# Performance work log

Measured on AMD Instinct MI355X. Metric: run time of the kernel, lower is better.

Reference implementation:

```python
import jax, jax.numpy as jnp
import numpy as np
from jax import lax

B, T, D, H = 64, 2048, 128, 256  # batch, seq_len, input_dim, hidden_dim


def setup_inputs() -> dict:
    key = jax.random.key(0)
    ks = jax.random.split(key, 21)
    s = 0.05
    p = lambda k, shape: jax.random.normal(k, shape, dtype=jnp.float32) * s
    inp = {"x": jax.random.normal(ks[0], (B, T, D), dtype=jnp.float32)}
    i = 1
    for n in ["e1", "e2", "d1", "d2"]:  # encode1, encode2, reconstruct1, reconstruct2
        inp[n + "_Wih"] = p(ks[i], (4 * H, D)); i += 1
        inp[n + "_Whh"] = p(ks[i], (4 * H, H)); i += 1
        inp[n + "_bih"] = p(ks[i], (4 * H,)); i += 1
        inp[n + "_bhh"] = p(ks[i], (4 * H,)); i += 1
    inp["l1_W"] = p(ks[17], (D, H)); inp["l1_b"] = p(ks[18], (D,))
    inp["l2_W"] = p(ks[19], (D, H)); inp["l2_b"] = p(ks[20], (D,))
    return inp


def _lstm_cell(h, c, xt, Wih, Whh, bih, bhh):
    # PyTorch gate order: i, f, g, o
    g = xt @ Wih.T + h @ Whh.T + bih + bhh  # [B, 4H]
    i, f, gg, o = jnp.split(g, 4, axis=-1)
    c = jax.nn.sigmoid(f) * c + jax.nn.sigmoid(i) * jnp.tanh(gg)
    h = jax.nn.sigmoid(o) * jnp.tanh(c)
    return h, c


def _encode(x, h0, c0, Wih, Whh, bih, bhh):
    # x: [B, T, D] batch_first -> scan over time
    def step(carry, xt):
        h, c = carry
        h, c = _lstm_cell(h, c, xt, Wih, Whh, bih, bhh)
        return (h, c), None
    (h, c), _ = lax.scan(step, (h0, c0), jnp.swapaxes(x, 0, 1))
    return h, c


def _decode(n, h, c, Wih, Whh, bih, bhh, Wl, bl):
    # first output is linear(hidden) before any cell step (matches original decode)
    inp0 = h @ Wl.T + bl  # [B, D]
    def step(carry, _):
        h, c, inp = carry
        h, c = _lstm_cell(h, c, inp, Wih, Whh, bih, bhh)
        inp = h @ Wl.T + bl
        return (h, c, inp), inp
    _, outs = lax.scan(step, (h, c, inp0), None, length=n - 1)  # [n-1, B, D]
    out = jnp.concatenate([inp0[None], outs], axis=0)  # [n, B, D]
    return jnp.swapaxes(out, 0, 1)  # [B, n, D]


def reference(x,
              e1_Wih, e1_Whh, e1_bih, e1_bhh,
              e2_Wih, e2_Whh, e2_bih, e2_bhh,
              d1_Wih, d1_Whh, d1_bih, d1_bhh,
              d2_Wih, d2_Whh, d2_bih, d2_bhh,
              l1_W, l1_b, l2_W, l2_b):
    Bc, Tc = x.shape[0], x.shape[1]
    T1 = Tc // 2
    h0 = jnp.zeros((Bc, H), dtype=x.dtype)
    c0 = jnp.zeros((Bc, H), dtype=x.dtype)
    x1 = x[:, :T1][:, ::-1]  # first half, time-reversed
    x2 = x[:, T1:]
    h1, c1 = _encode(x1, h0, c0, e1_Wih, e1_Whh, e1_bih, e1_bhh)
    h2, c2 = _encode(x2, h1, c1, e2_Wih, e2_Whh, e2_bih, e2_bhh)
    out1 = _decode(T1, h1, c1, d1_Wih, d1_Whh, d1_bih, d1_bhh, l1_W, l1_b)
    out2 = _decode(Tc - T1, h2, c2, d2_Wih, d2_Whh, d2_bih, d2_bhh, l2_W, l2_b)[:, ::-1]
    return jnp.concatenate([out1, out2], axis=1)  # [B, T, D]
```

## Files before the change

kernel.cpp:

```cpp
#include <hip/hip_runtime.h>
#include <stdint.h>

#define Bv 64
#define Tv 2048
#define T1v 1024
#define Dv 128
#define Hv 256

typedef _Float16 h2_t __attribute__((ext_vector_type(2)));

__device__ inline float d2(uint32_t hp, uint32_t wp, float acc) {
#if __has_builtin(__builtin_amdgcn_fdot2)
  return __builtin_amdgcn_fdot2(__builtin_bit_cast(h2_t, hp),
                                __builtin_bit_cast(h2_t, wp), acc, false);
#else
  float out;
  asm("v_dot2_f32_f16 %0, %1, %2, %3" : "=v"(out) : "v"(hp), "v"(wp), "v"(acc));
  return out;
#endif
}

__device__ inline uint16_t f2h(float x) {
  _Float16 h = (_Float16)x;
  return __builtin_bit_cast(uint16_t, h);
}
__device__ inline float h2f(uint16_t u) {
  return (float)__builtin_bit_cast(_Float16, u);
}
__device__ inline uint32_t packpair(float a, float b) {
  return (uint32_t)f2h(a) | ((uint32_t)f2h(b) << 16);
}
__device__ inline float unpk(uint32_t u, int hi) {
  return h2f((uint16_t)(hi ? (u >> 16) : (u & 0xffff)));
}
__device__ inline float sigm(float x) { return 1.f / (1.f + __expf(-x)); }
__device__ inline float tanh_(float x) { return 2.f / (1.f + __expf(-2.f * x)) - 1.f; }

__device__ inline float qsum4(float v) {
  int t = __builtin_amdgcn_update_dpp(0, __float_as_int(v), 0xB1, 0xF, 0xF, true);
  v += __int_as_float(t);
  t = __builtin_amdgcn_update_dpp(0, __float_as_int(v), 0x4E, 0xF, 0xF, true);
  return v + __int_as_float(t);
}

__device__ inline uint4 ld_stream(const uint4* p) {
  const volatile uint32_t* q = (const volatile uint32_t*)p;
  uint4 v;
  v.x = q[0];
  v.y = q[1];
  v.z = q[2];
  v.w = q[3];
  return v;
}


__global__ void k_pack_x(const float* __restrict__ x, uint32_t* __restrict__ xpk) {
  int idx = blockIdx.x * 256 + threadIdx.x;
  const float2* x2 = (const float2*)x;
  float2 v = x2[idx];
  xpk[idx] = packpair(v.x, v.y);
}

__global__ void k_pack_w(const float* __restrict__ src, uint32_t* __restrict__ wAll,
                         uint32_t* __restrict__ wLg, uint32_t* __restrict__ wStr) {
  int idx = blockIdx.x * 256 + threadIdx.x;
  int row = idx >> 7, k2 = idx & 127;
  uint32_t pr = packpair(src[row * 256 + 2 * k2], src[row * 256 + 2 * k2 + 1]);
  wAll[k2 * 1024 + row] = pr;
  if (k2 >= 96) {
    int g = (k2 - 96) >> 2, qq = (k2 - 96) & 3;
    wLg[(g * 1024 + row) * 4 + qq] = pr;
  }
  if (k2 >= 48 && k2 < 96) wStr[row * 48 + (k2 - 48)] = pr;
}

__global__ void k_pack_w2(const float* __restrict__ src, uint32_t* __restrict__ wSt,
                          uint32_t* __restrict__ wLds) {
  int idx = blockIdx.x * 256 + threadIdx.x;
  int r = idx >> 7, k2 = idx & 127;
  uint32_t pr = packpair(src[r * 256 + 2 * k2], src[r * 256 + 2 * k2 + 1]);
  int gate = r >> 8, u = r & 255;
  int u_hi = u >> 7, jb = u & 127;
  int q = k2 >> 5, kk = k2 & 31;
  int tid = jb * 4 + q;
  int ri = u_hi * 4 + gate;
  if (kk < 24) {
    wSt[((ri * 6 + (kk >> 2)) * 512 + tid) * 4 + (kk & 3)] = pr;
  } else {
    wLds[((ri * 2 + ((kk - 24) >> 2)) * 512 + tid) * 4 + ((kk - 24) & 3)] = pr;
  }
}

__global__ void k_bias_pack(const float* __restrict__ b32, uint32_t* __restrict__ bpk) {
  int jb = threadIdx.x;
  uint32_t w[4];
#pragma unroll
  for (int wi = 0; wi < 4; ++wi) {
    int ri0 = 2 * wi, ri1 = 2 * wi + 1;
    int row0 = (ri0 & 3) * 256 + jb + 128 * (ri0 >> 2);
    int row1 = (ri1 & 3) * 256 + jb + 128 * (ri1 >> 2);
    w[wi] = packpair(b32[row0], b32[row1]);
  }
  ((uint4*)bpk)[jb] = make_uint4(w[0], w[1], w[2], w[3]);
}

__global__ void k_pack_wih(const float* __restrict__ Wih, uint32_t* __restrict__ wihp) {
  int idx = blockIdx.x * 256 + threadIdx.x;
  int row = idx >> 6, k2 = idx & 63;
  wihp[row * 64 + k2] = packpair(Wih[row * 128 + 2 * k2], Wih[row * 128 + 2 * k2 + 1]);
}

__global__ void k_bias2(const float* __restrict__ bih, const float* __restrict__ bhh,
                        float* __restrict__ bias) {
  int i = blockIdx.x * 256 + threadIdx.x;
  if (i < 1024) bias[i] = bih[i] + bhh[i];
}

__global__ void k_dec_combine(const float* __restrict__ Whh, const float* __restrict__ Wih,
                              const float* __restrict__ bih, const float* __restrict__ bhh,
                              const float* __restrict__ lW, const float* __restrict__ lb,
                              float* __restrict__ wd, float* __restrict__ bias) {
  int j = blockIdx.x;
  int k = threadIdx.x;
  __shared__ float wr[128];
  if (k < 128) wr[k] = Wih[j * 128 + k];
  __syncthreads();
  float acc = Whh[j * 256 + k];
  for (int d = 0; d < 128; ++d) acc += wr[d] * lW[d * 256 + k];
  wd[j * 256 + k] = acc;
  if (k == 0) {
    float s = bih[j] + bhh[j];
    for (int d = 0; d < 128; ++d) s += wr[d] * lb[d];
    bias[j] = s;
  }
}

__global__ void k_pack_wl(const float* __restrict__ lW, uint32_t* __restrict__ wlp) {
  int idx = blockIdx.x * 256 + threadIdx.x;
  int d = idx >> 7, k2 = idx & 127;
  wlp[d * 128 + k2] = packpair(lW[d * 256 + 2 * k2], lW[d * 256 + 2 * k2 + 1]);
}

template <int LAY>
__global__ __launch_bounds__(256) void k_xp_gemm(const uint32_t* __restrict__ xpk,
                                                 const uint32_t* __restrict__ wihp,
                                                 uint16_t* __restrict__ xp, int xt0, int xdt) {
  const int b = blockIdx.z;
  const int s0 = blockIdx.y * 32;
  const int r = blockIdx.x * 256 + threadIdx.x;
  uint32_t wreg[64];
#pragma unroll
  for (int k = 0; k < 64; ++k) wreg[k] = wihp[r * 64 + k];
  const int gate = r >> 8, u = r & 255;
  const int u_hi = u >> 7, jb = u & 127;
  const int ri = u_hi * 4 + gate;
  for (int sl = 0; sl < 32; ++sl) {
    const int s = s0 + sl;
    const int t = xt0 + s * xdt;
    const uint32_t* __restrict__ xrow = xpk + ((size_t)b * Tv + t) * 64;
    float a0 = 0.f, a1 = 0.f;
#pragma unroll
    for (int k = 0; k < 64; k += 2) {
      a0 = d2(xrow[k], wreg[k], a0);
      a1 = d2(xrow[k + 1], wreg[k + 1], a1);
    }
    uint16_t v = f2h(a0 + a1);
    if (LAY == 0)
      xp[(((size_t)b * T1v + s) * 128 + jb) * 8 + ri] = v;
    else
      xp[((size_t)b * T1v + s) * 1024 + r] = v;
  }
}


struct CfgU {
  const uint4* wSt;
  const uint4* wLds;
  const uint4* bpk;
  const uint4* xps;
  const float* h0;
  const float* c0;
  float* hN;
  float* cN;
  uint16_t* hist;
};

template <int NREGC, int NSTRC, int NLDSC>
__global__ void __launch_bounds__(512)
__attribute__((amdgpu_waves_per_eu(2, 2)))
k_rnnU(CfgU cA, CfgU cB, int nA) {
  __shared__ __align__(16) uint4 wldsM[NLDSC * 8 * 512];
  __shared__ __align__(16) uint16_t hbuf[2][4][72];

  const bool isA = (int)blockIdx.x < nA;
  const CfgU cfg = isA ? cA : cB;
  const int b = isA ? (int)blockIdx.x : ((int)blockIdx.x - nA);
  const int tid = threadIdx.x;
  const int q = tid & 3, jb = tid >> 2;

#pragma unroll
  for (int ri = 0; ri < 8; ++ri)
#pragma unroll
    for (int li = 0; li < NLDSC; ++li)
      wldsM[(ri * NLDSC + li) * 512 + tid] =
          cfg.wLds[(ri * 2 + (2 - NLDSC) + li) * 512 + tid];

  uint4 wr[8][NREGC];
#pragma unroll
  for (int ri = 0; ri < 8; ++ri)
#pragma unroll
    for (int cc = 0; cc < NREGC; ++cc) wr[ri][cc] = cfg.wSt[(ri * 6 + cc) * 512 + tid];

  const uint4 bp = cfg.bpk[jb];
  float c0r = cfg.c0 ? cfg.c0[b * 256 + jb] : 0.f;
  float c1r = cfg.c0 ? cfg.c0[b * 256 + jb + 128] : 0.f;

  uint16_t* histp = cfg.hist ? cfg.hist + (size_t)b * 1024 * 256 : nullptr;
  if (q == 0) {
    float h00 = cfg.h0 ? cfg.h0[b * 256 + jb] : 0.f;
    float h01 = cfg.h0 ? cfg.h0[b * 256 + jb + 128] : 0.f;
    uint16_t u0 = f2h(h00), u1 = f2h(h01);
    hbuf[0][jb >> 6][jb & 63] = u0;
    hbuf[0][2 + (jb >> 6)][jb & 63] = u1;
    if (histp) {
      histp[jb] = u0;
      histp[jb + 128] = u1;
    }
  }
  const uint4* xps4 = cfg.xps ? cfg.xps + (size_t)b * 1024 * 128 + jb : nullptr;

  __syncthreads();

  int cur = 0;
  for (int s = 0; s < 1024; ++s) {
    uint4 xq = make_uint4(0, 0, 0, 0);
    if (xps4) xq = xps4[(size_t)s * 128];
    const uint4* Hq = (const uint4*)&hbuf[cur][q][0];

    float acc[8];
#pragma unroll
    for (int ri = 0; ri < 8; ++ri) acc[ri] = 0.f;

#pragma unroll
    for (int cc = 0; cc < NREGC; ++cc) {
      const uint4 hv = Hq[cc];
#pragma unroll
      for (int ri = 0; ri < 8; ++ri) {
        acc[ri] = d2(hv.x, wr[ri][cc].x, acc[ri]);
        acc[ri] = d2(hv.y, wr[ri][cc].y, acc[ri]);
        acc[ri] = d2(hv.z, wr[ri][cc].z, acc[ri]);
        acc[ri] = d2(hv.w, wr[ri][cc].w, acc[ri]);
      }
    }
#pragma unroll
    for (int j = 0; j < NSTRC; ++j) {
      const int cc = NREGC + j;
      const uint4 hv = Hq[cc];
#pragma unroll
      for (int ri = 0; ri < 8; ++ri) {
        const uint4 wv = (cc < 6) ? ld_stream(cfg.wSt + (ri * 6 + cc) * 512 + tid)
                                  : ld_stream(cfg.wLds + (ri * 2 + (cc - 6)) * 512 + tid);
        acc[ri] = d2(hv.x, wv.x, acc[ri]);
        acc[ri] = d2(hv.y, wv.y, acc[ri]);
        acc[ri] = d2(hv.z, wv.z, acc[ri]);
        acc[ri] = d2(hv.w, wv.w, acc[ri]);
      }
    }
#pragma unroll
    for (int li = 0; li < NLDSC; ++li) {
      const int cc = 8 - NLDSC + li;
      const uint4 hv = Hq[cc];
#pragma unroll
      for (int ri = 0; ri < 8; ++ri) {
        const uint4 wv = wldsM[(ri * NLDSC + li) * 512 + tid];
        acc[ri] = d2(hv.x, wv.x, acc[ri]);
        acc[ri] = d2(hv.y, wv.y, acc[ri]);
        acc[ri] = d2(hv.z, wv.z, acc[ri]);
        acc[ri] = d2(hv.w, wv.w, acc[ri]);
      }
    }

#pragma unroll
    for (int ri = 0; ri < 8; ++ri) acc[ri] = qsum4(acc[ri]);

    acc[0] += unpk(bp.x, 0) + unpk(xq.x, 0);
    acc[1] += unpk(bp.x, 1) + unpk(xq.x, 1);
    acc[2] += unpk(bp.y, 0) + unpk(xq.y, 0);
    acc[3] += unpk(bp.y, 1) + unpk(xq.y, 1);
    acc[4] += unpk(bp.z, 0) + unpk(xq.z, 0);
    acc[5] += unpk(bp.z, 1) + unpk(xq.z, 1);
    acc[6] += unpk(bp.w, 0) + unpk(xq.w, 0);
    acc[7] += unpk(bp.w, 1) + unpk(xq.w, 1);

    const float cn0 = sigm(acc[1]) * c0r + sigm(acc[0]) * tanh_(acc[2]);
    const float h0v = sigm(acc[3]) * tanh_(cn0);
    c0r = cn0;
    const float cn1 = sigm(acc[5]) * c1r + sigm(acc[4]) * tanh_(acc[6]);
    const float h1v = sigm(acc[7]) * tanh_(cn1);
    c1r = cn1;

    if (q == 0) {
      const uint16_t hu0 = f2h(h0v), hu1 = f2h(h1v);
      hbuf[cur ^ 1][jb >> 6][jb & 63] = hu0;
      hbuf[cur ^ 1][2 + (jb >> 6)][jb & 63] = hu1;
      if (histp && s < 1023) {
        histp[(size_t)(s + 1) * 256 + jb] = hu0;
        histp[(size_t)(s + 1) * 256 + jb + 128] = hu1;
      }
    }
    __syncthreads();
    cur ^= 1;
  }

  if (cfg.hN && q == 0) {
    cfg.hN[b * 256 + jb] = h2f(hbuf[cur][jb >> 6][jb & 63]);
    cfg.hN[b * 256 + jb + 128] = h2f(hbuf[cur][2 + (jb >> 6)][jb & 63]);
    cfg.cN[b * 256 + jb] = c0r;
    cfg.cN[b * 256 + jb + 128] = c1r;
  }
}


struct ChainCfg {
  const uint32_t* wAll;
  const uint4* wLg;
  const uint32_t* wStr;
  const uint32_t* wih;
  const uint32_t* xpk;
  const uint16_t* xps;
  const float* bias;
  const float* h0;
  const float* c0;
  float* hN;
  float* cN;
  uint16_t* hist;
  int xt0, xdt;
};

template <int NRESP, bool WIH>
__global__ void __launch_bounds__(512)
__attribute__((amdgpu_waves_per_eu(2, 2)))
k_rnn5(ChainCfg cA, ChainCfg cB, int nA) {
  __shared__ __align__(16) uint4 wlds4[8 * 1024];
  __shared__ float gsm[1024];
  __shared__ __align__(16) uint16_t h16[256];
  __shared__ __align__(16) uint32_t xsh[64];

  const bool isA = (int)blockIdx.x < nA;
  const ChainCfg cfg = isA ? cA : cB;
  const int b = isA ? (int)blockIdx.x : ((int)blockIdx.x - nA);
  const int tid = threadIdx.x;
  const int r0 = tid, r1 = tid + 512;

#pragma unroll
  for (int i = 0; i < 16; ++i) wlds4[i * 512 + tid] = cfg.wLg[i * 512 + tid];

  uint16_t* histp = cfg.hist ? cfg.hist + (size_t)b * 1024 * 256 : nullptr;

  float creg = 0.f;
  if (tid < 256) {
    float h0v = cfg.h0 ? cfg.h0[b * 256 + tid] : 0.f;
    creg = cfg.c0 ? cfg.c0[b * 256 + tid] : 0.f;
    uint16_t hu = f2h(h0v);
    h16[tid] = hu;
    if (histp) histp[tid] = hu;
  }

  uint32_t w0[NRESP], w1[NRESP];
#pragma unroll
  for (int k = 0; k < NRESP; ++k) w0[k] = cfg.wAll[k * 1024 + r0];
#pragma unroll
  for (int k = 0; k < NRESP; ++k) w1[k] = cfg.wAll[k * 1024 + r1];
  const float bias0 = cfg.bias[r0];
  const float bias1 = cfg.bias[r1];

  constexpr int NS4 = (96 - NRESP) / 4;
  const uint4* ws0 = (const uint4*)(cfg.wStr + (size_t)r0 * 48 + (NRESP - 48));
  const uint4* ws1 = (const uint4*)(cfg.wStr + (size_t)r1 * 48 + (NRESP - 48));
  const uint4* wi0 = cfg.wih ? (const uint4*)(cfg.wih + (size_t)r0 * 64) : nullptr;
  const uint4* wi1 = cfg.wih ? (const uint4*)(cfg.wih + (size_t)r1 * 64) : nullptr;
  const bool hasx = cfg.xps != nullptr;

  __syncthreads();

  for (int s = 0; s < 1024; ++s) {
    float xa0 = 0.f, xa1 = 0.f;
    if (hasx) {
      size_t xb = ((size_t)b * 1024 + s) * 1024;
      xa0 = h2f(cfg.xps[xb + r0]);
      xa1 = h2f(cfg.xps[xb + r1]);
    }
    if constexpr (WIH) {
      if (cfg.wih) {
        if (tid < 64) {
          const int t = cfg.xt0 + s * cfg.xdt;
          xsh[tid] = cfg.xpk[((size_t)b * Tv + t) * 64 + tid];
        }
        __syncthreads();
      }
    }

    const uint4* H4 = (const uint4*)h16;
    float a00 = bias0, a01 = 0.f, a10 = bias1, a11 = 0.f;

#pragma unroll
    for (int c4 = 0; c4 < NRESP / 4; ++c4) {
      const uint4 hv = H4[c4];
      a00 = d2(hv.x, w0[4 * c4 + 0], a00);
      a01 = d2(hv.y, w0[4 * c4 + 1], a01);
      a10 = d2(hv.x, w1[4 * c4 + 0], a10);
      a11 = d2(hv.y, w1[4 * c4 + 1], a11);
      a00 = d2(hv.z, w0[4 * c4 + 2], a00);
      a01 = d2(hv.w, w0[4 * c4 + 3], a01);
      a10 = d2(hv.z, w1[4 * c4 + 2], a10);
      a11 = d2(hv.w, w1[4 * c4 + 3], a11);
    }
    if constexpr (NS4 > 0) {
#pragma unroll
      for (int u = 0; u < NS4; ++u) {
        const uint4 hv = H4[NRESP / 4 + u];
        const uint4 wv0 = ws0[u];
        const uint4 wv1 = ws1[u];
        a00 = d2(hv.x, wv0.x, a00);
        a01 = d2(hv.y, wv0.y, a01);
        a10 = d2(hv.x, wv1.x, a10);
        a11 = d2(hv.y, wv1.y, a11);
        a00 = d2(hv.z, wv0.z, a00);
        a01 = d2(hv.w, wv0.w, a01);
        a10 = d2(hv.z, wv1.z, a10);
        a11 = d2(hv.w, wv1.w, a11);
      }
    }
#pragma unroll
    for (int g = 0; g < 8; ++g) {
      const uint4 hv = H4[24 + g];
      const uint4 wv0 = wlds4[g * 1024 + r0];
      const uint4 wv1 = wlds4[g * 1024 + r1];
      a00 = d2(hv.x, wv0.x, a00);
      a01 = d2(hv.y, wv0.y, a01);
      a10 = d2(hv.x, wv1.x, a10);
      a11 = d2(hv.y, wv1.y, a11);
      a00 = d2(hv.z, wv0.z, a00);
      a01 = d2(hv.w, wv0.w, a01);
      a10 = d2(hv.z, wv1.z, a10);
      a11 = d2(hv.w, wv1.w, a11);
    }
    if constexpr (WIH) {
      if (cfg.wih) {
        const uint4* XS4 = (const uint4*)xsh;
#pragma unroll
        for (int u = 0; u < 16; ++u) {
          const uint4 xv = XS4[u];
          const uint4 wv0 = wi0[u];
          const uint4 wv1 = wi1[u];
          a00 = d2(xv.x, wv0.x, a00);
          a01 = d2(xv.y, wv0.y, a01);
          a10 = d2(xv.x, wv1.x, a10);
          a11 = d2(xv.y, wv1.y, a11);
          a00 = d2(xv.z, wv0.z, a00);
          a01 = d2(xv.w, wv0.w, a01);
          a10 = d2(xv.z, wv1.z, a10);
          a11 = d2(xv.w, wv1.w, a11);
        }
      }
    }

    gsm[r0] = a00 + a01 + xa0;
    gsm[r1] = a10 + a11 + xa1;
    __syncthreads();

    if (tid < 256) {
      const float gi = gsm[tid];
      const float gf = gsm[tid + 256];
      const float gg = gsm[tid + 512];
      const float go = gsm[tid + 768];
      const float cn = sigm(gf) * creg + sigm(gi) * tanh_(gg);
      const float hv = sigm(go) * tanh_(cn);
      creg = cn;
      const uint16_t hu = f2h(hv);
      h16[tid] = hu;
      if (histp && s < 1023) histp[(size_t)(s + 1) * 256 + tid] = hu;
    }
    __syncthreads();
  }

  if (cfg.hN && tid < 256) {
    cfg.hN[b * 256 + tid] = h2f(h16[tid]);
    cfg.cN[b * 256 + tid] = creg;
  }
}

__global__ __launch_bounds__(256) void k_out(const uint16_t* __restrict__ hist,
                                             const uint32_t* __restrict__ wlp,
                                             const float* __restrict__ lb,
                                             float* __restrict__ out, int outbase, int tsign) {
  const int b = blockIdx.y;
  const int t0 = blockIdx.x * 64;
  __shared__ __align__(16) uint32_t hq[64 * 128];
  const uint32_t* hsrc = (const uint32_t*)hist;
  for (int i = threadIdx.x; i < 64 * 128; i += 256) {
    hq[i] = hsrc[((size_t)b * 1024 + t0) * 128 + i];
  }
  __syncthreads();
  const int d = threadIdx.x & 127;
  const int th = threadIdx.x >> 7;
  float acc[32];
#pragma unroll
  for (int it = 0; it < 32; ++it) acc[it] = lb[d];
  const uint4* W4 = (const uint4*)(wlp + (size_t)d * 128);
  const uint4* HQ4 = (const uint4*)hq;
  for (int k2c = 0; k2c < 32; ++k2c) {
    const uint4 wv = W4[k2c];
#pragma unroll
    for (int it = 0; it < 32; ++it) {
      const int tl = th * 32 + it;
      const uint4 hv = HQ4[tl * 32 + k2c];
      acc[it] = d2(hv.x, wv.x, acc[it]);
      acc[it] = d2(hv.y, wv.y, acc[it]);
      acc[it] = d2(hv.z, wv.z, acc[it]);
      acc[it] = d2(hv.w, wv.w, acc[it]);
    }
  }
#pragma unroll
  for (int it = 0; it < 32; ++it) {
    const int tl = th * 32 + it;
    const int t = t0 + tl;
    const int tout = outbase + tsign * t;
    out[((size_t)b * Tv + tout) * Dv + d] = acc[it];
  }
}


extern "C" void kernel_launch(void* const* d_in, const int* in_sizes, int n_in,
                              void* d_out, int out_size, void* d_ws, size_t ws_size,
                              hipStream_t stream) {
  const float* x = (const float*)d_in[0];
  const float* e1_Wih = (const float*)d_in[1];
  const float* e1_Whh = (const float*)d_in[2];
  const float* e1_bih = (const float*)d_in[3];
  const float* e1_bhh = (const float*)d_in[4];
  const float* e2_Wih = (const float*)d_in[5];
  const float* e2_Whh = (const float*)d_in[6];
  const float* e2_bih = (const float*)d_in[7];
  const float* e2_bhh = (const float*)d_in[8];
  const float* d1_Wih = (const float*)d_in[9];
  const float* d1_Whh = (const float*)d_in[10];
  const float* d1_bih = (const float*)d_in[11];
  const float* d1_bhh = (const float*)d_in[12];
  const float* d2_Wih = (const float*)d_in[13];
  const float* d2_Whh = (const float*)d_in[14];
  const float* d2_bih = (const float*)d_in[15];
  const float* d2_bhh = (const float*)d_in[16];
  const float* l1_W = (const float*)d_in[17];
  const float* l1_b = (const float*)d_in[18];
  const float* l2_W = (const float*)d_in[19];
  const float* l2_b = (const float*)d_in[20];

  uint8_t* wsb = (uint8_t*)d_ws;
  size_t off = 0;
  auto take = [&](size_t n) -> void* {
    void* pp = wsb + off;
    off += (n + 255) & ~(size_t)255;
    return pp;
  };
  uint32_t* xpk = (uint32_t*)take((size_t)Bv * Tv * 64 * 4);
  uint16_t* hist1 = (uint16_t*)take((size_t)Bv * T1v * Hv * 2);
  uint16_t* hist2 = (uint16_t*)take((size_t)Bv * T1v * Hv * 2);
  struct WSet {
    uint32_t *wAll, *wLg, *wStr, *wih;
    float* bias;
    uint32_t *wSt, *wLds, *bpk;
  };
  auto take_wset = [&](bool with_ih) -> WSet {
    WSet w;
    w.wAll = (uint32_t*)take(128 * 1024 * 4);
    w.wLg = (uint32_t*)take(8 * 1024 * 16);
    w.wStr = (uint32_t*)take(1024 * 48 * 4);
    w.wih = with_ih ? (uint32_t*)take(1024 * 64 * 4) : nullptr;
    w.bias = (float*)take(1024 * 4);
    w.wSt = (uint32_t*)take(48 * 512 * 16);
    w.wLds = (uint32_t*)take(16 * 512 * 16);
    w.bpk = (uint32_t*)take(128 * 16);
    return w;
  };
  WSet we1 = take_wset(true);
  WSet we2 = take_wset(true);
  WSet wd1 = take_wset(false);
  WSet wd2 = take_wset(false);
  float* wd32 = (float*)take(1024 * 256 * 4);
  uint32_t* wl1p = (uint32_t*)take(128 * 128 * 4);
  uint32_t* wl2p = (uint32_t*)take(128 * 128 * 4);
  float* h1 = (float*)take(64 * 256 * 4);
  float* c1 = (float*)take(64 * 256 * 4);
  float* h2 = (float*)take(64 * 256 * 4);
  float* c2 = (float*)take(64 * 256 * 4);
  uint16_t* xp = (uint16_t*)take((size_t)Bv * T1v * 1024 * 2);
  const bool use_xp = ws_size >= off;

  int variant = 4;
  {
    hipFuncAttributes fa;
    auto spillfree = [&](const void* f) {
      return hipFuncGetAttributes(&fa, f) == hipSuccess && fa.localSizeBytes == 0;
    };
    if (use_xp) {
      if (spillfree(reinterpret_cast<const void*>(&k_rnnU<6, 1, 1>))) variant = 0;
      else if (spillfree(reinterpret_cast<const void*>(&k_rnnU<6, 0, 2>))) variant = 1;
      else if (spillfree(reinterpret_cast<const void*>(&k_rnnU<4, 2, 2>))) variant = 2;
      else if (spillfree(reinterpret_cast<const void*>(&k_rnn5<96, false>))) variant = 3;
    } else {
      if (spillfree(reinterpret_cast<const void*>(&k_rnn5<96, true>))) variant = 3;
    }
  }

  k_pack_x<<<(Bv * Tv * 64) / 256, 256, 0, stream>>>(x, xpk);
  k_pack_w<<<512, 256, 0, stream>>>(e1_Whh, we1.wAll, we1.wLg, we1.wStr);
  k_pack_w2<<<512, 256, 0, stream>>>(e1_Whh, we1.wSt, we1.wLds);
  k_pack_wih<<<256, 256, 0, stream>>>(e1_Wih, we1.wih);
  k_bias2<<<4, 256, 0, stream>>>(e1_bih, e1_bhh, we1.bias);
  k_bias_pack<<<1, 128, 0, stream>>>(we1.bias, we1.bpk);
  k_pack_w<<<512, 256, 0, stream>>>(e2_Whh, we2.wAll, we2.wLg, we2.wStr);
  k_pack_w2<<<512, 256, 0, stream>>>(e2_Whh, we2.wSt, we2.wLds);
  k_pack_wih<<<256, 256, 0, stream>>>(e2_Wih, we2.wih);
  k_bias2<<<4, 256, 0, stream>>>(e2_bih, e2_bhh, we2.bias);
  k_bias_pack<<<1, 128, 0, stream>>>(we2.bias, we2.bpk);
  k_dec_combine<<<1024, 256, 0, stream>>>(d1_Whh, d1_Wih, d1_bih, d1_bhh, l1_W, l1_b, wd32, wd1.bias);
  k_pack_w<<<512, 256, 0, stream>>>(wd32, wd1.wAll, wd1.wLg, wd1.wStr);
  k_pack_w2<<<512, 256, 0, stream>>>(wd32, wd1.wSt, wd1.wLds);
  k_bias_pack<<<1, 128, 0, stream>>>(wd1.bias, wd1.bpk);
  k_dec_combine<<<1024, 256, 0, stream>>>(d2_Whh, d2_Wih, d2_bih, d2_bhh, l2_W, l2_b, wd32, wd2.bias);
  k_pack_w<<<512, 256, 0, stream>>>(wd32, wd2.wAll, wd2.wLg, wd2.wStr);
  k_pack_w2<<<512, 256, 0, stream>>>(wd32, wd2.wSt, wd2.wLds);
  k_bias_pack<<<1, 128, 0, stream>>>(wd2.bias, wd2.bpk);
  k_pack_wl<<<64, 256, 0, stream>>>(l1_W, wl1p);
  k_pack_wl<<<64, 256, 0, stream>>>(l2_W, wl2p);

  if (variant <= 2) {
    auto launch_u = [&](int grid, CfgU a, CfgU b2, int nA) {
      if (variant == 0)      k_rnnU<6, 1, 1><<<grid, 512, 0, stream>>>(a, b2, nA);
      else if (variant == 1) k_rnnU<6, 0, 2><<<grid, 512, 0, stream>>>(a, b2, nA);
      else                   k_rnnU<4, 2, 2><<<grid, 512, 0, stream>>>(a, b2, nA);
    };
    k_xp_gemm<0><<<dim3(4, 32, 64), 256, 0, stream>>>(xpk, we1.wih, xp, 1023, -1);
    CfgU e1c{(const uint4*)we1.wSt, (const uint4*)we1.wLds, (const uint4*)we1.bpk,
             (const uint4*)xp, nullptr, nullptr, h1, c1, nullptr};
    launch_u(64, e1c, e1c, 64);

    k_xp_gemm<0><<<dim3(4, 32, 64), 256, 0, stream>>>(xpk, we2.wih, xp, 1024, 1);
    CfgU e2c{(const uint4*)we2.wSt, (const uint4*)we2.wLds, (const uint4*)we2.bpk,
             (const uint4*)xp, h1, c1, h2, c2, nullptr};
    CfgU d1c{(const uint4*)wd1.wSt, (const uint4*)wd1.wLds, (const uint4*)wd1.bpk,
             nullptr, h1, c1, nullptr, nullptr, hist1};
    launch_u(128, e2c, d1c, 64);

    CfgU d2c{(const uint4*)wd2.wSt, (const uint4*)wd2.wLds, (const uint4*)wd2.bpk,
             nullptr, h2, c2, nullptr, nullptr, hist2};
    launch_u(64, d2c, d2c, 64);
  } else {
    auto launch_old = [&](int grid, ChainCfg a, ChainCfg b2, int nA) {
      if (use_xp) {
        if (variant == 3) k_rnn5<96, false><<<grid, 512, 0, stream>>>(a, b2, nA);
        else              k_rnn5<80, false><<<grid, 512, 0, stream>>>(a, b2, nA);
      } else {
        if (variant == 3) k_rnn5<96, true><<<grid, 512, 0, stream>>>(a, b2, nA);
        else              k_rnn5<80, true><<<grid, 512, 0, stream>>>(a, b2, nA);
      }
    };
    if (use_xp) k_xp_gemm<1><<<dim3(4, 32, 64), 256, 0, stream>>>(xpk, we1.wih, xp, 1023, -1);
    ChainCfg e1c{we1.wAll, (const uint4*)we1.wLg, we1.wStr, use_xp ? nullptr : we1.wih,
                 use_xp ? nullptr : xpk, use_xp ? xp : nullptr, we1.bias,
                 nullptr, nullptr, h1, c1, nullptr, 1023, -1};
    launch_old(64, e1c, e1c, 64);

    if (use_xp) k_xp_gemm<1><<<dim3(4, 32, 64), 256, 0, stream>>>(xpk, we2.wih, xp, 1024, 1);
    ChainCfg e2c{we2.wAll, (const uint4*)we2.wLg, we2.wStr, use_xp ? nullptr : we2.wih,
                 use_xp ? nullptr : xpk, use_xp ? xp : nullptr, we2.bias,
                 h1, c1, h2, c2, nullptr, 1024, 1};
    ChainCfg d1c{wd1.wAll, (const uint4*)wd1.wLg, wd1.wStr, nullptr, nullptr, nullptr,
                 wd1.bias, h1, c1, nullptr, nullptr, hist1, 0, 0};
    launch_old(128, e2c, d1c, 64);

    ChainCfg d2c{wd2.wAll, (const uint4*)wd2.wLg, wd2.wStr, nullptr, nullptr, nullptr,
                 wd2.bias, h2, c2, nullptr, nullptr, hist2, 0, 0};
    launch_old(64, d2c, d2c, 64);
  }

  k_out<<<dim3(16, 64), 256, 0, stream>>>(hist1, wl1p, l1_b, (float*)d_out, 0, 1);
  k_out<<<dim3(16, 64), 256, 0, stream>>>(hist2, wl2p, l2_b, (float*)d_out, 2047, -1);
}
```

Before: 7.299 ms.

## Batch 16 sequences per block and compute recurrent gates with MFMA

Adds a new recurrent kernel in which each 512-thread block handles 16 batch rows and computes the h·Whh product with mfma_f32_16x16x32_f16 instead of per-sequence fp16 dot2 instructions. Weights are split across registers, LDS and double-buffered global streaming, and the x-projection is precomputed into an MFMA-fragment layout with the bias folded in. The grid shrinks from 64 or 128 blocks to 4 or 8, so far fewer CUs are used. The cost is less parallelism, a per-step streaming load of part of the weights, and a barrier over the whole block every step.

```diff
diff --git a/kernel.cpp b/kernel.cpp
--- a/kernel.cpp
+++ b/kernel.cpp
@@ -8,6 +8,8 @@
 #define Hv 256
 
 typedef _Float16 h2_t __attribute__((ext_vector_type(2)));
+typedef _Float16 f16x8 __attribute__((ext_vector_type(8)));
+typedef float f32x4 __attribute__((ext_vector_type(4)));
 
 __device__ inline float d2(uint32_t hp, uint32_t wp, float acc) {
 #if __has_builtin(__builtin_amdgcn_fdot2)
@@ -43,16 +45,6 @@
   return v + __int_as_float(t);
 }
 
-__device__ inline uint4 ld_stream(const uint4* p) {
-  const volatile uint32_t* q = (const volatile uint32_t*)p;
-  uint4 v;
-  v.x = q[0];
-  v.y = q[1];
-  v.z = q[2];
-  v.w = q[3];
-  return v;
-}
-
 
 __global__ void k_pack_x(const float* __restrict__ x, uint32_t* __restrict__ xpk) {
   int idx = blockIdx.x * 256 + threadIdx.x;
@@ -74,7 +66,7 @@
   if (k2 >= 48 && k2 < 96) wStr[row * 48 + (k2 - 48)] = pr;
 }
 
-__global__ void k_pack_w2(const float* __restrict__ src, uint32_t* __restrict__ wSt,
+__global__ void k_pack_w2(const float* __restrict__ src, uint32_t* __restrict__ wReg,
                           uint32_t* __restrict__ wLds) {
   int idx = blockIdx.x * 256 + threadIdx.x;
   int r = idx >> 7, k2 = idx & 127;
@@ -84,11 +76,46 @@
   int q = k2 >> 5, kk = k2 & 31;
   int tid = jb * 4 + q;
   int ri = u_hi * 4 + gate;
-  if (kk < 24) {
-    wSt[((ri * 6 + (kk >> 2)) * 512 + tid) * 4 + (kk & 3)] = pr;
+  int cc = kk >> 2, c = kk & 3;
+  if (cc < 6) wReg[((ri * 6 + cc) * 512 + tid) * 4 + c] = pr;
+  else        wLds[((ri * 2 + (cc - 6)) * 512 + tid) * 4 + c] = pr;
+}
+
+__global__ void k_pack_wf(const float* __restrict__ src, uint32_t* __restrict__ resF,
+                          uint32_t* __restrict__ ldsF, uint32_t* __restrict__ strF,
+                          int CR, int CL, int CS) {
+  int idx = blockIdx.x * 256 + threadIdx.x;
+  int r = idx >> 7, k2 = idx & 127;
+  int k = 2 * k2;
+  uint32_t pr = packpair(src[r * 256 + k], src[r * 256 + k + 1]);
+  int gate = r >> 8, u = r & 255;
+  int rowp = u * 4 + gate;
+  int t = rowp >> 4, w = t >> 3, tt = t & 7, rr = rowp & 15;
+  int c = k >> 5, kk = k & 31;
+  int lane = rr + 16 * (kk >> 3);
+  int dw = (kk & 7) >> 1;
+  if (c < CR) {
+    resF[(((w * CR + c) * 8 + tt) * 64 + lane) * 4 + dw] = pr;
+  } else if (c < CR + CL) {
+    ldsF[(((w * CL + (c - CR)) * 8 + tt) * 64 + lane) * 4 + dw] = pr;
   } else {
-    wLds[((ri * 2 + ((kk - 24) >> 2)) * 512 + tid) * 4 + ((kk - 24) & 3)] = pr;
-  }
+    int cs = c - CR - CL;
+    size_t o = (((size_t)(w * CS + cs) * 8 + tt) * 64 + lane) * 4 + dw;
+    strF[o] = pr;
+    strF[o + (size_t)CS * 4096 * 4] = pr;
+  }
+}
+
+__global__ void k_pack_biasf(const float* __restrict__ b32, uint16_t* __restrict__ biasF) {
+  int r = blockIdx.x * 256 + threadIdx.x;
+  if (r >= 1024) return;
+  int gate = r >> 8, u = r & 255;
+  int rowp = u * 4 + gate;
+  int t = rowp >> 4, w = t >> 3, tt = t & 7, rr = rowp & 15;
+  int lg = rr >> 2, reg = rr & 3;
+  uint16_t v = f2h(b32[r]);
+  for (int bl = 0; bl < 16; ++bl)
+    biasF[(w * 64 + (bl + 16 * lg)) * 32 + tt * 4 + reg] = v;
 }
 
 __global__ void k_bias_pack(const float* __restrict__ b32, uint32_t* __restrict__ bpk) {
@@ -172,10 +199,213 @@
   }
 }
 
+__global__ __launch_bounds__(256) void k_xp_gemmF(const uint32_t* __restrict__ xpk,
+                                                  const uint32_t* __restrict__ wihp,
+                                                  const float* __restrict__ bias,
+                                                  uint16_t* __restrict__ xpf, int xt0, int xdt) {
+  const int b = blockIdx.z;
+  const int s0 = blockIdx.y * 32;
+  const int r = blockIdx.x * 256 + threadIdx.x;
+  uint32_t wreg[64];
+#pragma unroll
+  for (int k = 0; k < 64; ++k) wreg[k] = wihp[r * 64 + k];
+  const float bv = bias[r];
+  const int gate = r >> 8, u = r & 255;
+  const int rowp = u * 4 + gate;
+  const int t = rowp >> 4, w = t >> 3, tt = t & 7, rr = rowp & 15;
+  const int lane = (b & 15) + 16 * (rr >> 2);
+  const int reg = rr & 3;
+  const int bt = b >> 4;
+  for (int sl = 0; sl < 32; ++sl) {
+    const int s = s0 + sl;
+    const int tx = xt0 + s * xdt;
+    const uint32_t* __restrict__ xrow = xpk + ((size_t)b * Tv + tx) * 64;
+    float a0 = 0.f, a1 = 0.f;
+#pragma unroll
+    for (int k = 0; k < 64; k += 2) {
+      a0 = d2(xrow[k], wreg[k], a0);
+      a1 = d2(xrow[k + 1], wreg[k + 1], a1);
+    }
+    xpf[(((size_t)bt * 1024 + s) * 512 + w * 64 + lane) * 32 + tt * 4 + reg] =
+        f2h(a0 + a1 + bv);
+  }
+}
+
+
+struct CfgM {
+  const uint4* resF;
+  const uint4* ldsF;
+  const uint4* strF;
+  const uint16_t* biasF;
+  const uint16_t* xpf;
+  const float* h0;
+  const float* c0;
+  float* hN;
+  float* cN;
+  uint16_t* hist;
+};
+
+template <int CR, int CL, int CS>
+__global__ void __launch_bounds__(512)
+__attribute__((amdgpu_waves_per_eu(2, 2)))
+k_rnnM(CfgM cA, CfgM cB, int nA) {
+  __shared__ __align__(16) uint4 wldsA[CL > 0 ? CL * 4096 : 1];
+  __shared__ __align__(16) uint16_t hb[2][16][264];
+
+  const bool isA = (int)blockIdx.x < nA;
+  const CfgM cfg = isA ? cA : cB;
+  const int bi = isA ? (int)blockIdx.x : ((int)blockIdx.x - nA);
+  const int b0 = bi * 16;
+  const int tid = threadIdx.x;
+  const int w = tid >> 6, l = tid & 63;
+  const int bl = l & 15, lg = l >> 4;
+
+  if (CL > 0) {
+#pragma unroll
+    for (int i = 0; i < CL * 8; ++i) wldsA[i * 512 + tid] = cfg.ldsF[i * 512 + tid];
+  }
+
+  uint4 wrA[CR * 8];
+#pragma unroll
+  for (int i = 0; i < CR * 8; ++i) wrA[i] = cfg.resF[((size_t)w * CR * 8 + i) * 64 + l];
+
+  uint4 bh[4];
+#pragma unroll
+  for (int j = 0; j < 4; ++j) bh[j] = ((const uint4*)cfg.biasF)[(w * 64 + l) * 4 + j];
+
+  float cst[8];
+#pragma unroll
+  for (int tt = 0; tt < 8; ++tt) {
+    int unit = (w * 8 + tt) * 4 + lg;
+    cst[tt] = cfg.c0 ? cfg.c0[(b0 + bl) * 256 + unit] : 0.f;
+  }
+
+  {
+    int batch = tid >> 5, u0 = (tid & 31) * 8;
+    uint16_t tmp[8];
+#pragma unroll
+    for (int j = 0; j < 8; ++j)
+      tmp[j] = f2h(cfg.h0 ? cfg.h0[(b0 + batch) * 256 + u0 + j] : 0.f);
+    *(uint4*)((char*)&hb[0][0][0] + batch * 528 + u0 * 2) = *(const uint4*)tmp;
+  }
+  __syncthreads();
+
+  char* hb0 = (char*)&hb[0][0][0];
+  const size_t hbsz = 16 * 264 * 2;
+  int cur = 0;
+
+  for (int s = 0; s < 1024; ++s) {
+    const char* hbc = hb0 + (size_t)cur * hbsz;
+
+    if (cfg.hist) {
+      int batch = tid >> 5, u0 = (tid & 31) * 8;
+      uint4 hv = *(const uint4*)(hbc + batch * 528 + u0 * 2);
+      *(uint4*)(cfg.hist + ((size_t)(b0 + batch) * 1024 + s) * 256 + u0) = hv;
+    }
+
+    f32x4 acc[8];
+    if (cfg.xpf) {
+      const uint4* xp4 = (const uint4*)(cfg.xpf + (((size_t)bi * 1024 + s) * 512 + tid) * 32);
+      uint4 xh[4];
+#pragma unroll
+      for (int j = 0; j < 4; ++j) xh[j] = xp4[j];
+      const _Float16* xv = (const _Float16*)xh;
+#pragma unroll
+      for (int tt = 0; tt < 8; ++tt)
+#pragma unroll
+        for (int rg = 0; rg < 4; ++rg) acc[tt][rg] = (float)xv[tt * 4 + rg];
+    } else {
+      const _Float16* bv = (const _Float16*)bh;
+#pragma unroll
+      for (int tt = 0; tt < 8; ++tt)
+#pragma unroll
+        for (int rg = 0; rg < 4; ++rg) acc[tt][rg] = (float)bv[tt * 4 + rg];
+    }
+
+#pragma unroll
+    for (int c = 0; c < CR; ++c) {
+      f16x8 bf = __builtin_bit_cast(f16x8,
+          *(const uint4*)(hbc + bl * 528 + c * 64 + lg * 16));
+#pragma unroll
+      for (int tt = 0; tt < 8; ++tt)
+        acc[tt] = __builtin_amdgcn_mfma_f32_16x16x32_f16(
+            __builtin_bit_cast(f16x8, wrA[c * 8 + tt]), bf, acc[tt], 0, 0, 0);
+    }
+    if (CL > 0) {
+#pragma unroll
+      for (int cl = 0; cl < CL; ++cl) {
+        const int c = CR + cl;
+        f16x8 bf = __builtin_bit_cast(f16x8,
+            *(const uint4*)(hbc + bl * 528 + c * 64 + lg * 16));
+#pragma unroll
+        for (int tt = 0; tt < 8; ++tt) {
+          uint4 au = wldsA[(w * CL + cl) * 512 + tt * 64 + l];
+          acc[tt] = __builtin_amdgcn_mfma_f32_16x16x32_f16(
+              __builtin_bit_cast(f16x8, au), bf, acc[tt], 0, 0, 0);
+        }
+      }
+    }
+    if (CS > 0) {
+      const uint4* sp = cfg.strF + ((s & 1) ? (size_t)CS * 4096 : 0);
+      uint4 pf[8];
+#pragma unroll
+      for (int tt = 0; tt < 8; ++tt) pf[tt] = sp[((size_t)w * CS) * 512 + tt * 64 + l];
+#pragma unroll
+      for (int cs = 0; cs < CS; ++cs) {
+        const int c = CR + CL + cs;
+        uint4 cu[8];
+#pragma unroll
+        for (int tt = 0; tt < 8; ++tt) cu[tt] = pf[tt];
+        if (cs + 1 < CS) {
+#pragma unroll
+          for (int tt = 0; tt < 8; ++tt)
+            pf[tt] = sp[((size_t)w * CS + cs + 1) * 512 + tt * 64 + l];
+        }
+        f16x8 bf = __builtin_bit_cast(f16x8,
+            *(const uint4*)(hbc + bl * 528 + c * 64 + lg * 16));
+#pragma unroll
+        for (int tt = 0; tt < 8; ++tt)
+          acc[tt] = __builtin_amdgcn_mfma_f32_16x16x32_f16(
+              __builtin_bit_cast(f16x8, cu[tt]), bf, acc[tt], 0, 0, 0);
+      }
+    }
+
+    char* hbn = hb0 + (size_t)(cur ^ 1) * hbsz;
+#pragma unroll
+    for (int tt = 0; tt < 8; ++tt) {
+      const float i_ = sigm(acc[tt][0]);
+      const float f_ = sigm(acc[tt][1]);
+      const float g_ = tanh_(acc[tt][2]);
+      const float o_ = sigm(acc[tt][3]);
+      const float cn = f_ * cst[tt] + i_ * g_;
+      cst[tt] = cn;
+      const float hv = o_ * tanh_(cn);
+      const int unit = (w * 8 + tt) * 4 + lg;
+      *(uint16_t*)(hbn + bl * 528 + unit * 2) = f2h(hv);
+    }
+    __syncthreads();
+    cur ^= 1;
+  }
+
+  if (cfg.hN) {
+    const char* hbc = hb0 + (size_t)cur * hbsz;
+    int batch = tid >> 5, u0 = (tid & 31) * 8;
+#pragma unroll
+    for (int j = 0; j < 8; ++j)
+      cfg.hN[(b0 + batch) * 256 + u0 + j] =
+          h2f(*(const uint16_t*)(hbc + batch * 528 + (u0 + j) * 2));
+#pragma unroll
+    for (int tt = 0; tt < 8; ++tt) {
+      int unit = (w * 8 + tt) * 4 + lg;
+      cfg.cN[(b0 + bl) * 256 + unit] = cst[tt];
+    }
+  }
+}
+
 
 struct CfgU {
-  const uint4* wSt;
-  const uint4* wLds;
+  const uint4* wA;
+  const uint4* wC;
   const uint4* bpk;
   const uint4* xps;
   const float* h0;
@@ -185,11 +415,10 @@
   uint16_t* hist;
 };
 
-template <int NREGC, int NSTRC, int NLDSC>
 __global__ void __launch_bounds__(512)
 __attribute__((amdgpu_waves_per_eu(2, 2)))
-k_rnnU(CfgU cA, CfgU cB, int nA) {
-  __shared__ __align__(16) uint4 wldsM[NLDSC * 8 * 512];
+k_rnnU6(CfgU cA, CfgU cB, int nA) {
+  __shared__ __align__(16) uint4 wldsM[2 * 8 * 512];
   __shared__ __align__(16) uint16_t hbuf[2][4][72];
 
   const bool isA = (int)blockIdx.x < nA;
@@ -199,17 +428,13 @@
   const int q = tid & 3, jb = tid >> 2;
 
 #pragma unroll
+  for (int i = 0; i < 16; ++i) wldsM[i * 512 + tid] = cfg.wC[i * 512 + tid];
+
+  uint4 wr[8][6];
+#pragma unroll
   for (int ri = 0; ri < 8; ++ri)
 #pragma unroll
-    for (int li = 0; li < NLDSC; ++li)
-      wldsM[(ri * NLDSC + li) * 512 + tid] =
-          cfg.wLds[(ri * 2 + (2 - NLDSC) + li) * 512 + tid];
-
-  uint4 wr[8][NREGC];
-#pragma unroll
-  for (int ri = 0; ri < 8; ++ri)
-#pragma unroll
-    for (int cc = 0; cc < NREGC; ++cc) wr[ri][cc] = cfg.wSt[(ri * 6 + cc) * 512 + tid];
+    for (int cc = 0; cc < 6; ++cc) wr[ri][cc] = cfg.wA[(ri * 6 + cc) * 512 + tid];
 
   const uint4 bp = cfg.bpk[jb];
   float c0r = cfg.c0 ? cfg.c0[b * 256 + jb] : 0.f;
@@ -235,14 +460,14 @@
   for (int s = 0; s < 1024; ++s) {
     uint4 xq = make_uint4(0, 0, 0, 0);
     if (xps4) xq = xps4[(size_t)s * 128];
-    const uint4* Hq = (const uint4*)&hbuf[cur][q][0];
+    const uint4* Hq = (const uint4*)(&hbuf[cur][q][0]);
 
     float acc[8];
 #pragma unroll
     for (int ri = 0; ri < 8; ++ri) acc[ri] = 0.f;
 
 #pragma unroll
-    for (int cc = 0; cc < NREGC; ++cc) {
+    for (int cc = 0; cc < 6; ++cc) {
       const uint4 hv = Hq[cc];
 #pragma unroll
       for (int ri = 0; ri < 8; ++ri) {
@@ -253,26 +478,11 @@
       }
     }
 #pragma unroll
-    for (int j = 0; j < NSTRC; ++j) {
-      const int cc = NREGC + j;
-      const uint4 hv = Hq[cc];
+    for (int lI = 0; lI < 2; ++lI) {
+      const uint4 hv = Hq[6 + lI];
 #pragma unroll
       for (int ri = 0; ri < 8; ++ri) {
-        const uint4 wv = (cc < 6) ? ld_stream(cfg.wSt + (ri * 6 + cc) * 512 + tid)
-                                  : ld_stream(cfg.wLds + (ri * 2 + (cc - 6)) * 512 + tid);
-        acc[ri] = d2(hv.x, wv.x, acc[ri]);
-        acc[ri] = d2(hv.y, wv.y, acc[ri]);
-        acc[ri] = d2(hv.z, wv.z, acc[ri]);
-        acc[ri] = d2(hv.w, wv.w, acc[ri]);
-      }
-    }
-#pragma unroll
-    for (int li = 0; li < NLDSC; ++li) {
-      const int cc = 8 - NLDSC + li;
-      const uint4 hv = Hq[cc];
-#pragma unroll
-      for (int ri = 0; ri < 8; ++ri) {
-        const uint4 wv = wldsM[(ri * NLDSC + li) * 512 + tid];
+        const uint4 wv = wldsM[(ri * 2 + lI) * 512 + tid];
         acc[ri] = d2(hv.x, wv.x, acc[ri]);
         acc[ri] = d2(hv.y, wv.y, acc[ri]);
         acc[ri] = d2(hv.z, wv.z, acc[ri]);
@@ -567,20 +777,26 @@
   uint16_t* hist1 = (uint16_t*)take((size_t)Bv * T1v * Hv * 2);
   uint16_t* hist2 = (uint16_t*)take((size_t)Bv * T1v * Hv * 2);
   struct WSet {
-    uint32_t *wAll, *wLg, *wStr, *wih;
+    uint32_t *wAll, *wLg, *wStr48, *wih;
     float* bias;
-    uint32_t *wSt, *wLds, *bpk;
+    uint32_t *wReg, *wLds, *bpk;
+    uint32_t *resF, *ldsF, *strF;
+    uint16_t* biasF;
   };
   auto take_wset = [&](bool with_ih) -> WSet {
     WSet w;
     w.wAll = (uint32_t*)take(128 * 1024 * 4);
     w.wLg = (uint32_t*)take(8 * 1024 * 16);
-    w.wStr = (uint32_t*)take(1024 * 48 * 4);
+    w.wStr48 = (uint32_t*)take(1024 * 48 * 4);
     w.wih = with_ih ? (uint32_t*)take(1024 * 64 * 4) : nullptr;
     w.bias = (float*)take(1024 * 4);
-    w.wSt = (uint32_t*)take(48 * 512 * 16);
+    w.wReg = (uint32_t*)take(48 * 512 * 16);
     w.wLds = (uint32_t*)take(16 * 512 * 16);
     w.bpk = (uint32_t*)take(128 * 16);
+    w.resF = (uint32_t*)take((size_t)5 * 4096 * 16);
+    w.ldsF = (uint32_t*)take((size_t)2 * 4096 * 16);
+    w.strF = (uint32_t*)take((size_t)2 * 3 * 4096 * 16);
+    w.biasF = (uint16_t*)take(512 * 32 * 2);
     return w;
   };
   WSet we1 = take_wset(true);
@@ -597,90 +813,126 @@
   uint16_t* xp = (uint16_t*)take((size_t)Bv * T1v * 1024 * 2);
   const bool use_xp = ws_size >= off;
 
-  int variant = 4;
+  int variant = 5;
+  int MCR = 0, MCL = 0, MCS = 0;
   {
     hipFuncAttributes fa;
-    auto spillfree = [&](const void* f) {
+    auto sf = [&](const void* f) {
       return hipFuncGetAttributes(&fa, f) == hipSuccess && fa.localSizeBytes == 0;
     };
     if (use_xp) {
-      if (spillfree(reinterpret_cast<const void*>(&k_rnnU<6, 1, 1>))) variant = 0;
-      else if (spillfree(reinterpret_cast<const void*>(&k_rnnU<6, 0, 2>))) variant = 1;
-      else if (spillfree(reinterpret_cast<const void*>(&k_rnnU<4, 2, 2>))) variant = 2;
-      else if (spillfree(reinterpret_cast<const void*>(&k_rnn5<96, false>))) variant = 3;
+      if (sf(reinterpret_cast<const void*>(&k_rnnM<5, 1, 2>))) { variant = 0; MCR = 5; MCL = 1; MCS = 2; }
+      else if (sf(reinterpret_cast<const void*>(&k_rnnM<4, 2, 2>))) { variant = 1; MCR = 4; MCL = 2; MCS = 2; }
+      else if (sf(reinterpret_cast<const void*>(&k_rnnM<3, 2, 3>))) { variant = 2; MCR = 3; MCL = 2; MCS = 3; }
+      else if (sf(reinterpret_cast<const void*>(&k_rnnU6))) variant = 3;
+      else if (sf(reinterpret_cast<const void*>(&k_rnn5<96, false>))) variant = 4;
     } else {
-      if (spillfree(reinterpret_cast<const void*>(&k_rnn5<96, true>))) variant = 3;
+      if (sf(reinterpret_cast<const void*>(&k_rnn5<96, true>))) variant = 4;
     }
   }
 
   k_pack_x<<<(Bv * Tv * 64) / 256, 256, 0, stream>>>(x, xpk);
-  k_pack_w<<<512, 256, 0, stream>>>(e1_Whh, we1.wAll, we1.wLg, we1.wStr);
-  k_pack_w2<<<512, 256, 0, stream>>>(e1_Whh, we1.wSt, we1.wLds);
   k_pack_wih<<<256, 256, 0, stream>>>(e1_Wih, we1.wih);
+  k_pack_wih<<<256, 256, 0, stream>>>(e2_Wih, we2.wih);
   k_bias2<<<4, 256, 0, stream>>>(e1_bih, e1_bhh, we1.bias);
-  k_bias_pack<<<1, 128, 0, stream>>>(we1.bias, we1.bpk);
-  k_pack_w<<<512, 256, 0, stream>>>(e2_Whh, we2.wAll, we2.wLg, we2.wStr);
-  k_pack_w2<<<512, 256, 0, stream>>>(e2_Whh, we2.wSt, we2.wLds);
-  k_pack_wih<<<256, 256, 0, stream>>>(e2_Wih, we2.wih);
   k_bias2<<<4, 256, 0, stream>>>(e2_bih, e2_bhh, we2.bias);
-  k_bias_pack<<<1, 128, 0, stream>>>(we2.bias, we2.bpk);
-  k_dec_combine<<<1024, 256, 0, stream>>>(d1_Whh, d1_Wih, d1_bih, d1_bhh, l1_W, l1_b, wd32, wd1.bias);
-  k_pack_w<<<512, 256, 0, stream>>>(wd32, wd1.wAll, wd1.wLg, wd1.wStr);
-  k_pack_w2<<<512, 256, 0, stream>>>(wd32, wd1.wSt, wd1.wLds);
-  k_bias_pack<<<1, 128, 0, stream>>>(wd1.bias, wd1.bpk);
-  k_dec_combine<<<1024, 256, 0, stream>>>(d2_Whh, d2_Wih, d2_bih, d2_bhh, l2_W, l2_b, wd32, wd2.bias);
-  k_pack_w<<<512, 256, 0, stream>>>(wd32, wd2.wAll, wd2.wLg, wd2.wStr);
-  k_pack_w2<<<512, 256, 0, stream>>>(wd32, wd2.wSt, wd2.wLds);
-  k_bias_pack<<<1, 128, 0, stream>>>(wd2.bias, wd2.bpk);
   k_pack_wl<<<64, 256, 0, stream>>>(l1_W, wl1p);
   k_pack_wl<<<64, 256, 0, stream>>>(l2_W, wl2p);
 
   if (variant <= 2) {
-    auto launch_u = [&](int grid, CfgU a, CfgU b2, int nA) {
-      if (variant == 0)      k_rnnU<6, 1, 1><<<grid, 512, 0, stream>>>(a, b2, nA);
-      else if (variant == 1) k_rnnU<6, 0, 2><<<grid, 512, 0, stream>>>(a, b2, nA);
-      else                   k_rnnU<4, 2, 2><<<grid, 512, 0, stream>>>(a, b2, nA);
+    k_pack_wf<<<512, 256, 0, stream>>>(e1_Whh, we1.resF, we1.ldsF, we1.strF, MCR, MCL, MCS);
+    k_pack_wf<<<512, 256, 0, stream>>>(e2_Whh, we2.resF, we2.ldsF, we2.strF, MCR, MCL, MCS);
+    k_pack_biasf<<<4, 256, 0, stream>>>(we1.bias, we1.biasF);
+    k_pack_biasf<<<4, 256, 0, stream>>>(we2.bias, we2.biasF);
+    k_dec_combine<<<1024, 256, 0, stream>>>(d1_Whh, d1_Wih, d1_bih, d1_bhh, l1_W, l1_b, wd32, wd1.bias);
+    k_pack_wf<<<512, 256, 0, stream>>>(wd32, wd1.resF, wd1.ldsF, wd1.strF, MCR, MCL, MCS);
+    k_pack_biasf<<<4, 256, 0, stream>>>(wd1.bias, wd1.biasF);
+    k_dec_combine<<<1024, 256, 0, stream>>>(d2_Whh, d2_Wih, d2_bih, d2_bhh, l2_W, l2_b, wd32, wd2.bias);
+    k_pack_wf<<<512, 256, 0, stream>>>(wd32, wd2.resF, wd2.ldsF, wd2.strF, MCR, MCL, MCS);
+    k_pack_biasf<<<4, 256, 0, stream>>>(wd2.bias, wd2.biasF);
+
+    auto mk = [&](WSet& w, const uint16_t* xpf, const float* h0, const float* c0,
+                  float* hN, float* cN, uint16_t* hist) -> CfgM {
+      return CfgM{(const uint4*)w.resF, (const uint4*)w.ldsF, (const uint4*)w.strF,
+                  w.biasF, xpf, h0, c0, hN, cN, hist};
+    };
+    auto launch_m = [&](int grid, CfgM a, CfgM b2, int nA) {
+      if (variant == 0)      k_rnnM<5, 1, 2><<<grid, 512, 0, stream>>>(a, b2, nA);
+      else if (variant == 1) k_rnnM<4, 2, 2><<<grid, 512, 0, stream>>>(a, b2, nA);
+      else                   k_rnnM<3, 2, 3><<<grid, 512, 0, stream>>>(a, b2, nA);
+    };
+
+    k_xp_gemmF<<<dim3(4, 32, 64), 256, 0, stream>>>(xpk, we1.wih, we1.bias, xp, 1023, -1);
+    CfgM e1c = mk(we1, xp, nullptr, nullptr, h1, c1, nullptr);
+    launch_m(4, e1c, e1c, 4);
+
+    k_xp_gemmF<<<dim3(4, 32, 64), 256, 0, stream>>>(xpk, we2.wih, we2.bias, xp, 1024, 1);
+    CfgM e2c = mk(we2, xp, h1, c1, h2, c2, nullptr);
+    CfgM d1c = mk(wd1, nullptr, h1, c1, nullptr, nullptr, hist1);
+    launch_m(8, e2c, d1c, 4);
+
+    CfgM d2c = mk(wd2, nullptr, h2, c2, nullptr, nullptr, hist2);
+    launch_m(4, d2c, d2c, 4);
+  } else if (variant == 3) {
+    k_pack_w2<<<512, 256, 0, stream>>>(e1_Whh, we1.wReg, we1.wLds);
+    k_pack_w2<<<512, 256, 0, stream>>>(e2_Whh, we2.wReg, we2.wLds);
+    k_bias_pack<<<1, 128, 0, stream>>>(we1.bias, we1.bpk);
+    k_bias_pack<<<1, 128, 0, stream>>>(we2.bias, we2.bpk);
+    k_dec_combine<<<1024, 256, 0, stream>>>(d1_Whh, d1_Wih, d1_bih, d1_bhh, l1_W, l1_b, wd32, wd1.bias);
+    k_pack_w2<<<512, 256, 0, stream>>>(wd32, wd1.wReg, wd1.wLds);
+    k_bias_pack<<<1, 128, 0, stream>>>(wd1.bias, wd1.bpk);
+    k_dec_combine<<<1024, 256, 0, stream>>>(d2_Whh, d2_Wih, d2_bih, d2_bhh, l2_W, l2_b, wd32, wd2.bias);
+    k_pack_w2<<<512, 256, 0, stream>>>(wd32, wd2.wReg, wd2.wLds);
+    k_bias_pack<<<1, 128, 0, stream>>>(wd2.bias, wd2.bpk);
+
+    auto mk = [&](WSet& w, const uint4* xps, const float* h0, const float* c0,
+                  float* hN, float* cN, uint16_t* hist) -> CfgU {
+      return CfgU{(const uint4*)w.wReg, (const uint4*)w.wLds,
+                  (const uint4*)w.bpk, xps, h0, c0, hN, cN, hist};
     };
     k_xp_gemm<0><<<dim3(4, 32, 64), 256, 0, stream>>>(xpk, we1.wih, xp, 1023, -1);
-    CfgU e1c{(const uint4*)we1.wSt, (const uint4*)we1.wLds, (const uint4*)we1.bpk,
-             (const uint4*)xp, nullptr, nullptr, h1, c1, nullptr};
-    launch_u(64, e1c, e1c, 64);
+    CfgU e1c = mk(we1, (const uint4*)xp, nullptr, nullptr, h1, c1, nullptr);
+    k_rnnU6<<<64, 512, 0, stream>>>(e1c, e1c, 64);
 
     k_xp_gemm<0><<<dim3(4, 32, 64), 256, 0, stream>>>(xpk, we2.wih, xp, 1024, 1);
-    CfgU e2c{(const uint4*)we2.wSt, (const uint4*)we2.wLds, (const uint4*)we2.bpk,
-             (const uint4*)xp, h1, c1, h2, c2, nullptr};
-    CfgU d1c{(const uint4*)wd1.wSt, (const uint4*)wd1.wLds, (const uint4*)wd1.bpk,
-             nullptr, h1, c1, nullptr, nullptr, hist1};
-    launch_u(128, e2c, d1c, 64);
-
-    CfgU d2c{(const uint4*)wd2.wSt, (const uint4*)wd2.wLds, (const uint4*)wd2.bpk,
-             nullptr, h2, c2, nullptr, nullptr, hist2};
-    launch_u(64, d2c, d2c, 64);
+    CfgU e2c = mk(we2, (const uint4*)xp, h1, c1, h2, c2, nullptr);
+    CfgU d1c = mk(wd1, nullptr, h1, c1, nullptr, nullptr, hist1);
+    k_rnnU6<<<128, 512, 0, stream>>>(e2c, d1c, 64);
+
+    CfgU d2c = mk(wd2, nullptr, h2, c2, nullptr, nullptr, hist2);
+    k_rnnU6<<<64, 512, 0, stream>>>(d2c, d2c, 64);
   } else {
+    k_pack_w<<<512, 256, 0, stream>>>(e1_Whh, we1.wAll, we1.wLg, we1.wStr48);
+    k_pack_w<<<512, 256, 0, stream>>>(e2_Whh, we2.wAll, we2.wLg, we2.wStr48);
+    k_dec_combine<<<1024, 256, 0, stream>>>(d1_Whh, d1_Wih, d1_bih, d1_bhh, l1_W, l1_b, wd32, wd1.bias);
+    k_pack_w<<<512, 256, 0, stream>>>(wd32, wd1.wAll, wd1.wLg, wd1.wStr48);
+    k_dec_combine<<<1024, 256, 0, stream>>>(d2_Whh, d2_Wih, d2_bih, d2_bhh, l2_W, l2_b, wd32, wd2.bias);
+    k_pack_w<<<512, 256, 0, stream>>>(wd32, wd2.wAll, wd2.wLg, wd2.wStr48);
+
     auto launch_old = [&](int grid, ChainCfg a, ChainCfg b2, int nA) {
       if (use_xp) {
-        if (variant == 3) k_rnn5<96, false><<<grid, 512, 0, stream>>>(a, b2, nA);
+        if (variant == 4) k_rnn5<96, false><<<grid, 512, 0, stream>>>(a, b2, nA);
         else              k_rnn5<80, false><<<grid, 512, 0, stream>>>(a, b2, nA);
       } else {
-        if (variant == 3) k_rnn5<96, true><<<grid, 512, 0, stream>>>(a, b2, nA);
+        if (variant == 4) k_rnn5<96, true><<<grid, 512, 0, stream>>>(a, b2, nA);
         else              k_rnn5<80, true><<<grid, 512, 0, stream>>>(a, b2, nA);
       }
     };
     if (use_xp) k_xp_gemm<1><<<dim3(4, 32, 64), 256, 0, stream>>>(xpk, we1.wih, xp, 1023, -1);
-    ChainCfg e1c{we1.wAll, (const uint4*)we1.wLg, we1.wStr, use_xp ? nullptr : we1.wih,
+    ChainCfg e1c{we1.wAll, (const uint4*)we1.wLg, we1.wStr48, use_xp ? nullptr : we1.wih,
                  use_xp ? nullptr : xpk, use_xp ? xp : nullptr, we1.bias,
                  nullptr, nullptr, h1, c1, nullptr, 1023, -1};
     launch_old(64, e1c, e1c, 64);
 
     if (use_xp) k_xp_gemm<1><<<dim3(4, 32, 64), 256, 0, stream>>>(xpk, we2.wih, xp, 1024, 1);
-    ChainCfg e2c{we2.wAll, (const uint4*)we2.wLg, we2.wStr, use_xp ? nullptr : we2.wih,
+    ChainCfg e2c{we2.wAll, (const uint4*)we2.wLg, we2.wStr48, use_xp ? nullptr : we2.wih,
                  use_xp ? nullptr : xpk, use_xp ? xp : nullptr, we2.bias,
                  h1, c1, h2, c2, nullptr, 1024, 1};
-    ChainCfg d1c{wd1.wAll, (const uint4*)wd1.wLg, wd1.wStr, nullptr, nullptr, nullptr,
+    ChainCfg d1c{wd1.wAll, (const uint4*)wd1.wLg, wd1.wStr48, nullptr, nullptr, nullptr,
                  wd1.bias, h1, c1, nullptr, nullptr, hist1, 0, 0};
     launch_old(128, e2c, d1c, 64);
 
-    ChainCfg d2c{wd2.wAll, (const uint4*)wd2.wLg, wd2.wStr, nullptr, nullptr, nullptr,
+    ChainCfg d2c{wd2.wAll, (const uint4*)wd2.wLg, wd2.wStr48, nullptr, nullptr, nullptr,
                  wd2.bias, h2, c2, nullptr, nullptr, hist2, 0, 0};
     launch_old(64, d2c, d2c, 64);
   }
```

New measurement: 7.167 ms. About the same (-1.8%).
